# Kernel tuning notes

Hardware: AMD Instinct MI355X
Metric: run time of the kernel (lower is better)

The kernel has to match this reference:

```python
import jax, jax.numpy as jnp
import numpy as np

WEIGHT = 1e-7
SIGMA_RGB = 15.0
SIGMA_XY = 100.0
SCALE = 0.5


def _nearest_resize(x, Ho, Wo):
    # torch F.interpolate mode='nearest': src = floor(dst * in/out)
    H, W = x.shape[-2], x.shape[-1]
    iy = (jnp.arange(Ho) * (H / Ho)).astype(jnp.int32)
    ix = (jnp.arange(Wo) * (W / Wo)).astype(jnp.int32)
    return x[..., iy[:, None], ix[None, :]]


def _bilinear_resize(x, Ho, Wo):
    # torch bilinear, align_corners=False (half-pixel centers, no antialias)
    H, W = x.shape[-2], x.shape[-1]
    yc = jnp.clip((jnp.arange(Ho, dtype=jnp.float32) + 0.5) * (H / Ho) - 0.5, 0.0, H - 1.0)
    xc = jnp.clip((jnp.arange(Wo, dtype=jnp.float32) + 0.5) * (W / Wo) - 0.5, 0.0, W - 1.0)
    y0 = jnp.floor(yc).astype(jnp.int32); y1 = jnp.minimum(y0 + 1, H - 1); ty = yc - y0
    x0 = jnp.floor(xc).astype(jnp.int32); x1 = jnp.minimum(x0 + 1, W - 1); tx = xc - x0
    g = lambda yi, xi: x[..., yi[:, None], xi[None, :]]
    top = g(y0, x0) * (1.0 - tx) + g(y0, x1) * tx
    bot = g(y1, x0) * (1.0 - tx) + g(y1, x1) * tx
    return top * (1.0 - ty[:, None]) + bot * ty[:, None]


def _dense_energy(images, segmentations, ROIs, seg_label):
    N, K, H, W = segmentations.shape
    Ho, Wo = int(H * SCALE), int(W * SCALE)
    P = Ho * Wo
    img_s = _nearest_resize(images, Ho, Wo)            # [N,3,Ho,Wo]
    seg_s = _bilinear_resize(segmentations, Ho, Wo)    # [N,K,Ho,Wo]
    roi_s = _nearest_resize(ROIs, Ho, Wo)              # [N,Ho,Wo]
    lbl_s = _nearest_resize(seg_label, Ho, Wo)         # [N,1,Ho,Wo]
    unlabel = (lbl_s == 255)[:, 0]                     # [N,Ho,Wo]

    # Gate = clamp(ROI - max_k seg, min=0), with unlabeled region forced to 1
    gate = roi_s - jnp.max(seg_s, axis=1)
    gate = jnp.where(unlabel, 1.0, gate)
    gate = jnp.maximum(gate, 0.0)
    gate = jax.lax.stop_gradient(gate)                 # constant in the custom backward

    seg_roi = seg_s * roi_s[:, None]                   # [N,K,Ho,Wo]

    sxy = SIGMA_XY * SCALE
    yy, xx = jnp.meshgrid(jnp.arange(Ho, dtype=jnp.float32),
                          jnp.arange(Wo, dtype=jnp.float32), indexing='ij')
    pos = jnp.stack([xx.ravel() / sxy, yy.ravel() / sxy], axis=-1)  # [P,2]

    def per_image(img, seg):
        # img [3,Ho,Wo], seg [K,Ho,Wo] -> AS [K,P]: Gaussian bilateral filter
        col = img.reshape(img.shape[0], P).T / SIGMA_RGB            # [P,3]
        f = jnp.concatenate([pos, col], axis=-1)                    # [P,5]
        sq = jnp.sum(f * f, axis=-1)
        d2 = jnp.maximum(sq[:, None] + sq[None, :] - 2.0 * (f @ f.T), 0.0)
        Wm = jnp.exp(-0.5 * d2)                                     # [P,P] affinity
        return seg.reshape(seg.shape[0], P) @ Wm                    # symmetric Wm

    AS = jax.vmap(per_image)(img_s, seg_roi)                        # [N,K,P]
    AS = AS * gate.reshape(N, 1, P)
    loss = -jnp.sum(seg_roi.reshape(N, K, P) * AS) / N
    return (WEIGHT * loss).reshape(1)


def setup_inputs() -> dict:
    key = jax.random.key(0)
    k1, k2, k3, k4 = jax.random.split(key, 4)
    N, C, K, H, W = 4, 3, 21, 128, 128
    images = jax.random.uniform(k1, (N, C, H, W), dtype=jnp.float32) * 255.0
    segmentations = jax.nn.softmax(jax.random.normal(k2, (N, K, H, W), dtype=jnp.float32), axis=1)
    ROIs = jax.random.randint(k3, (N, H, W), 0, 2).astype(jnp.float32)
    seg_label = jax.random.randint(k4, (N, 1, H, W), 0, 256).astype(jnp.int32)
    return {"images": images, "segmentations": segmentations, "ROIs": ROIs, "seg_label": seg_label}


def reference(images, segmentations, ROIs, seg_label):
    return _dense_energy(images, segmentations, ROIs, seg_label)
```

## Files before the change

kernel.cpp:

```cpp
#include <hip/hip_runtime.h>
#include <hip/hip_bf16.h>


typedef _Float16 v8h __attribute__((ext_vector_type(8)));
typedef float v16f __attribute__((ext_vector_type(16)));

#define NIMG 4
#define KCH 21
#define HIN 128
#define WIN 128
#define PPX 4096

#define SG_OFF   0x000000
#define SR_OFF   0x0C0000
#define FT_OFF   0x180000
#define SQ_OFF   0x200000
#define PART_OFF 0x210000

#define CEXP -0.72134752044448170f
#define M2C   1.44269504088896341f

__device__ __forceinline__ float fexp2(float x) {
#if __has_builtin(__builtin_amdgcn_exp2f)
    return __builtin_amdgcn_exp2f(x);
#else
    return __expf(x * 0.69314718055994531f);
#endif
}

__global__ __launch_bounds__(256) void prep_kernel(
    const float* __restrict__ img, const float* __restrict__ seg,
    const float* __restrict__ roi, const int* __restrict__ lbl,
    char* __restrict__ ws)
{
    int gid = blockIdx.x * 256 + threadIdx.x;
    int n = gid >> 12, p = gid & (PPX - 1);
    int y = p >> 6, x = p & 63, iy = 2 * y, ix = 2 * x;
    const float inv_rgb = 1.0f / 15.0f, inv_sxy = 1.0f / 50.0f;

    float rv = roi[((size_t)n * HIN + iy) * WIN + ix];
    int   lb = lbl[((size_t)n * HIN + iy) * WIN + ix];

    float sv[KCH]; float maxs = 0.0f;
    #pragma unroll
    for (int k = 0; k < KCH; k++) {
        const float* sp = seg + ((((size_t)n * KCH + k) * HIN + iy) * WIN + ix);
        float2 a = *(const float2*)sp;
        float2 c = *(const float2*)(sp + WIN);
        float s = 0.25f * (a.x + a.y + c.x + c.y);
        maxs = fmaxf(maxs, s);
        sv[k] = s * rv;
    }
    float gate = (lb == 255) ? 1.0f : fmaxf(rv - maxs, 0.0f);

    union { v8h h[3]; _Float16 e[24]; } rr, gg;
    #pragma unroll
    for (int k = 0; k < KCH; k++) {
        rr.e[k] = (_Float16)sv[k];
        gg.e[k] = (_Float16)(sv[k] * gate);
    }
    #pragma unroll
    for (int k = KCH; k < 24; k++) { rr.e[k] = (_Float16)0.f; gg.e[k] = (_Float16)0.f; }

    v8h* sgp = (v8h*)(ws + SG_OFF + (size_t)gid * 48);
    v8h* srp = (v8h*)(ws + SR_OFF + (size_t)gid * 48);
    sgp[0] = gg.h[0]; sgp[1] = gg.h[1]; sgp[2] = gg.h[2];
    srp[0] = rr.h[0]; srp[1] = rr.h[1]; srp[2] = rr.h[2];

    float f[5];
    f[0] = (float)x * inv_sxy;
    f[1] = (float)y * inv_sxy;
    f[2] = img[(((size_t)n * 3 + 0) * HIN + iy) * WIN + ix] * inv_rgb;
    f[3] = img[(((size_t)n * 3 + 1) * HIN + iy) * WIN + ix] * inv_rgb;
    f[4] = img[(((size_t)n * 3 + 2) * HIN + iy) * WIN + ix] * inv_rgb;

    union { v8h h[2]; _Float16 e[16]; } ff;
    float sq = 0.f;
    #pragma unroll
    for (int i = 0; i < 5; i++) {
        _Float16 hi = (_Float16)f[i];
        _Float16 lo = (_Float16)(f[i] - (float)hi);
        ff.e[i] = hi; ff.e[8 + i] = lo;
        float fe = (float)hi + (float)lo;
        sq = fmaf(fe, fe, sq);
    }
    #pragma unroll
    for (int i = 5; i < 8; i++) { ff.e[i] = (_Float16)0.f; ff.e[8 + i] = (_Float16)0.f; }

    v8h* ftp = (v8h*)(ws + FT_OFF + (size_t)gid * 32);
    ftp[0] = ff.h[0]; ftp[1] = ff.h[1];
    *(float*)(ws + SQ_OFF + (size_t)gid * 4) = CEXP * sq;
}

#define QS_O 0
#define QF_O 9216
#define QQ_O 14336
#define PS_O 14848
#define PF_O 24064
#define PQ_O 29184
#define RED_O 29696
#define LDS_BYTES 29712

__global__ __launch_bounds__(256) void pairs_kernel(
    const char* __restrict__ ws, float* __restrict__ part)
{
    __shared__ __align__(16) char smem[LDS_BYTES];
    int b = blockIdx.x;
    int ps = b & 7, qt = (b >> 3) & 31, n = b >> 8;
    int t = threadIdx.x;
    int lane = t & 63, half = lane >> 5, lr = lane & 31, wv = t >> 6;
    int wq = wv & 1, wp = wv >> 1;

    const float* SGg = (const float*)(ws + SG_OFF);
    const float* SRg = (const float*)(ws + SR_OFF);
    const float* FTg = (const float*)(ws + FT_OFF);
    const float* SQg = (const float*)(ws + SQ_OFF);

    if (t < 128) {
        *(float2*)(smem + QS_O + t * 72 + 48) = make_float2(0.f, 0.f);
        *(float2*)(smem + QS_O + t * 72 + 56) = make_float2(0.f, 0.f);
        *(float2*)(smem + PS_O + t * 72 + 48) = make_float2(0.f, 0.f);
        *(float2*)(smem + PS_O + t * 72 + 56) = make_float2(0.f, 0.f);
    }

    {
        int qbase = n * PPX + qt * 128;
        const float* gS = SRg + (size_t)qbase * 12;
        #pragma unroll
        for (int i = 0; i < 6; i++) {
            int d = t + i * 256;
            int row = d / 12, off = d - row * 12;
            *(float*)(smem + QS_O + row * 72 + off * 4) = gS[d];
        }
        const float* gF = FTg + (size_t)qbase * 8;
        #pragma unroll
        for (int i = 0; i < 4; i++) {
            int d = t + i * 256;
            int row = d >> 3, off = d & 7;
            *(float*)(smem + QF_O + row * 40 + off * 4) = gF[d];
        }
        if (t < 128) *(float*)(smem + QQ_O + t * 4) = SQg[qbase + t];
    }
    __syncthreads();

    v8h BS[2][2], BFH[2], BFL[2]; float sqq[2];
    #pragma unroll
    for (int s = 0; s < 2; s++) {
        int cr = wq * 64 + s * 32 + lr;
        const char* rb = smem + QS_O + cr * 72 + half * 16;
        union { v8h h; float2 f[2]; } u0, u1, uh, ul;
        u0.f[0] = *(const float2*)(rb);        u0.f[1] = *(const float2*)(rb + 8);
        u1.f[0] = *(const float2*)(rb + 32);   u1.f[1] = *(const float2*)(rb + 40);
        const char* fb = smem + QF_O + cr * 40;
        uh.f[0] = *(const float2*)(fb);        uh.f[1] = *(const float2*)(fb + 8);
        ul.f[0] = *(const float2*)(fb + 16);   ul.f[1] = *(const float2*)(fb + 24);
        BS[s][0] = u0.h; BS[s][1] = u1.h; BFH[s] = uh.h; BFL[s] = ul.h;
        sqq[s] = *(const float*)(smem + QQ_O + cr * 4);
    }

    float a0c = 0.f, a1c = 0.f, a2c = 0.f, a3c = 0.f;
    int pbase0 = n * PPX + ps * 512;

    for (int ch = 0; ch < 4; ch++) {
        __syncthreads();
        int pbase = pbase0 + ch * 128;
        const float* gS = SGg + (size_t)pbase * 12;
        #pragma unroll
        for (int i = 0; i < 6; i++) {
            int d = t + i * 256;
            int row = d / 12, off = d - row * 12;
            *(float*)(smem + PS_O + row * 72 + off * 4) = gS[d];
        }
        const float* gF = FTg + (size_t)pbase * 8;
        #pragma unroll
        for (int i = 0; i < 4; i++) {
            int d = t + i * 256;
            int row = d >> 3, off = d & 7;
            *(float*)(smem + PF_O + row * 40 + off * 4) = gF[d];
        }
        if (t < 128) *(float*)(smem + PQ_O + t * 4) = SQg[pbase + t];
        __syncthreads();

        #pragma unroll
        for (int sp = 0; sp < 2; sp++) {
            int pr = wp * 64 + sp * 32 + lr;
            union { v8h h; float2 f[2]; } a0, a1, af;
            const char* rb = smem + PS_O + pr * 72 + half * 16;
            a0.f[0] = *(const float2*)(rb);        a0.f[1] = *(const float2*)(rb + 8);
            a1.f[0] = *(const float2*)(rb + 32);   a1.f[1] = *(const float2*)(rb + 40);
            const char* fb2 = smem + PF_O + pr * 40 + half * 16;
            af.f[0] = *(const float2*)(fb2);       af.f[1] = *(const float2*)(fb2 + 8);

            float sqp[16];
            int pr0 = wp * 64 + sp * 32 + half * 4;
            #pragma unroll
            for (int r = 0; r < 16; r++) {
                int row = pr0 + (r & 3) + 8 * (r >> 2);
                sqp[r] = *(const float*)(smem + PQ_O + row * 4);
            }

            #pragma unroll
            for (int s = 0; s < 2; s++) {
                v16f z = {0.f,0.f,0.f,0.f,0.f,0.f,0.f,0.f,0.f,0.f,0.f,0.f,0.f,0.f,0.f,0.f};
                v16f c2 = __builtin_amdgcn_mfma_f32_32x32x16_f16(af.h, BFH[s], z, 0, 0, 0);
                c2 = __builtin_amdgcn_mfma_f32_32x32x16_f16(af.h, BFL[s], c2, 0, 0, 0);
                v16f c1 = __builtin_amdgcn_mfma_f32_32x32x16_f16(a0.h, BS[s][0], z, 0, 0, 0);
                c1 = __builtin_amdgcn_mfma_f32_32x32x16_f16(a1.h, BS[s][1], c1, 0, 0, 0);
                float sqv = sqq[s];
                #pragma unroll
                for (int r = 0; r < 16; r++) {
                    float arg = fmaf(M2C, c2[r], sqp[r] + sqv);
                    arg = fminf(arg, 0.0f);
                    float w = fexp2(arg);
                    float v = w * c1[r];
                    if ((r & 3) == 0) a0c += v;
                    else if ((r & 3) == 1) a1c += v;
                    else if ((r & 3) == 2) a2c += v;
                    else a3c += v;
                }
            }
        }
    }

    float acc = (a0c + a1c) + (a2c + a3c);
    #pragma unroll
    for (int off = 32; off > 0; off >>= 1) acc += __shfl_down(acc, off, 64);
    float* wred = (float*)(smem + RED_O);
    if ((t & 63) == 0) wred[t >> 6] = acc;
    __syncthreads();
    if (t == 0)
        part[blockIdx.x] = (wred[0] + wred[1]) + (wred[2] + wred[3]);
}

__global__ __launch_bounds__(256) void finalize_kernel(
    const float* __restrict__ part, float* __restrict__ out)
{
    __shared__ float s[256];
    int t = threadIdx.x;
    float v = ((part[t] + part[t + 256]) + (part[t + 512] + part[t + 768]));
    s[t] = v;
    __syncthreads();
    #pragma unroll
    for (int off = 128; off > 0; off >>= 1) {
        if (t < off) s[t] += s[t + off];
        __syncthreads();
    }
    if (t == 0) out[0] = s[0] * (-1e-7f / (float)NIMG);
}

extern "C" void kernel_launch(void* const* d_in, const int* in_sizes, int n_in,
                              void* d_out, int out_size, void* d_ws, size_t ws_size,
                              hipStream_t stream) {
    const float* images = (const float*)d_in[0];
    const float* seg    = (const float*)d_in[1];
    const float* rois   = (const float*)d_in[2];
    const int*   lbl    = (const int*)d_in[3];
    float* out = (float*)d_out;
    char*  ws  = (char*)d_ws;
    float* part = (float*)(ws + PART_OFF);

    hipLaunchKernelGGL(prep_kernel, dim3((NIMG * PPX) / 256), dim3(256), 0, stream,
                       images, seg, rois, lbl, ws);
    hipLaunchKernelGGL(pairs_kernel, dim3(NIMG * 32 * 8), dim3(256), 0, stream,
                       (const char*)ws, part);
    hipLaunchKernelGGL(finalize_kernel, dim3(1), dim3(256), 0, stream,
                       (const float*)part, out);
}
```

Measured before the change: 90.74 us.

## Exploit affinity symmetry with upper-triangular tiles and fuse final reduction

The pairs kernel now walks only the upper-triangular 128x128 tile pairs of the symmetric affinity matrix. The gate factor is moved inside the sum as (g_p + g_q), and diagonal tiles are halved, which cuts exp and MFMA work roughly in half. Prep writes one packed 128-byte record per pixel instead of separate gated and ungated segmentation arrays. The separate finalize kernel is replaced by a last-block-done atomic counter reduction. The cost is more LDS per block, a triangular index loop per block, and reliance on counter-based cross-block synchronization.

```diff
diff --git a/kernel.cpp b/kernel.cpp
--- a/kernel.cpp
+++ b/kernel.cpp
@@ -10,12 +10,12 @@
 #define HIN 128
 #define WIN 128
 #define PPX 4096
-
-#define SG_OFF   0x000000
-#define SR_OFF   0x0C0000
-#define FT_OFF   0x180000
-#define SQ_OFF   0x200000
-#define PART_OFF 0x210000
+#define TPB 32
+#define TRI 528
+#define NBLK (NIMG * TRI)
+
+#define PART_OFF 0x200000
+#define CNT_OFF  0x202200
 
 #define CEXP -0.72134752044448170f
 #define M2C   1.44269504088896341f
@@ -34,6 +34,7 @@
     char* __restrict__ ws)
 {
     int gid = blockIdx.x * 256 + threadIdx.x;
+    if (gid == 0) *(unsigned*)(ws + CNT_OFF) = 0u;
     int n = gid >> 12, p = gid & (PPX - 1);
     int y = p >> 6, x = p & 63, iy = 2 * y, ix = 2 * x;
     const float inv_rgb = 1.0f / 15.0f, inv_sxy = 1.0f / 50.0f;
@@ -41,7 +42,9 @@
     float rv = roi[((size_t)n * HIN + iy) * WIN + ix];
     int   lb = lbl[((size_t)n * HIN + iy) * WIN + ix];
 
-    float sv[KCH]; float maxs = 0.0f;
+    union { float4 q[8]; float f[32]; _Float16 e[64]; } rec;
+
+    float maxs = 0.0f;
     #pragma unroll
     for (int k = 0; k < KCH; k++) {
         const float* sp = seg + ((((size_t)n * KCH + k) * HIN + iy) * WIN + ix);
@@ -49,23 +52,12 @@
         float2 c = *(const float2*)(sp + WIN);
         float s = 0.25f * (a.x + a.y + c.x + c.y);
         maxs = fmaxf(maxs, s);
-        sv[k] = s * rv;
-    }
+        rec.e[k] = (_Float16)(s * rv);
+    }
+    #pragma unroll
+    for (int k = KCH; k < 32; k++) rec.e[k] = (_Float16)0.f;
+
     float gate = (lb == 255) ? 1.0f : fmaxf(rv - maxs, 0.0f);
-
-    union { v8h h[3]; _Float16 e[24]; } rr, gg;
-    #pragma unroll
-    for (int k = 0; k < KCH; k++) {
-        rr.e[k] = (_Float16)sv[k];
-        gg.e[k] = (_Float16)(sv[k] * gate);
-    }
-    #pragma unroll
-    for (int k = KCH; k < 24; k++) { rr.e[k] = (_Float16)0.f; gg.e[k] = (_Float16)0.f; }
-
-    v8h* sgp = (v8h*)(ws + SG_OFF + (size_t)gid * 48);
-    v8h* srp = (v8h*)(ws + SR_OFF + (size_t)gid * 48);
-    sgp[0] = gg.h[0]; sgp[1] = gg.h[1]; sgp[2] = gg.h[2];
-    srp[0] = rr.h[0]; srp[1] = rr.h[1]; srp[2] = rr.h[2];
 
     float f[5];
     f[0] = (float)x * inv_sxy;
@@ -74,150 +66,137 @@
     f[3] = img[(((size_t)n * 3 + 1) * HIN + iy) * WIN + ix] * inv_rgb;
     f[4] = img[(((size_t)n * 3 + 2) * HIN + iy) * WIN + ix] * inv_rgb;
 
-    union { v8h h[2]; _Float16 e[16]; } ff;
     float sq = 0.f;
     #pragma unroll
     for (int i = 0; i < 5; i++) {
         _Float16 hi = (_Float16)f[i];
         _Float16 lo = (_Float16)(f[i] - (float)hi);
-        ff.e[i] = hi; ff.e[8 + i] = lo;
+        rec.e[32 + i] = hi; rec.e[40 + i] = lo;
         float fe = (float)hi + (float)lo;
         sq = fmaf(fe, fe, sq);
     }
     #pragma unroll
-    for (int i = 5; i < 8; i++) { ff.e[i] = (_Float16)0.f; ff.e[8 + i] = (_Float16)0.f; }
-
-    v8h* ftp = (v8h*)(ws + FT_OFF + (size_t)gid * 32);
-    ftp[0] = ff.h[0]; ftp[1] = ff.h[1];
-    *(float*)(ws + SQ_OFF + (size_t)gid * 4) = CEXP * sq;
-}
-
-#define QS_O 0
-#define QF_O 9216
-#define QQ_O 14336
-#define PS_O 14848
-#define PF_O 24064
-#define PQ_O 29184
-#define RED_O 29696
-#define LDS_BYTES 29712
-
-__global__ __launch_bounds__(256) void pairs_kernel(
-    const char* __restrict__ ws, float* __restrict__ part)
+    for (int i = 5; i < 8; i++) { rec.e[32 + i] = (_Float16)0.f; rec.e[40 + i] = (_Float16)0.f; }
+
+    rec.f[24] = CEXP * sq;
+    rec.f[25] = gate;
+    rec.f[26] = 0.f; rec.f[27] = 0.f;
+    rec.f[28] = 0.f; rec.f[29] = 0.f; rec.f[30] = 0.f; rec.f[31] = 0.f;
+
+    float4* dst = (float4*)(ws + (size_t)gid * 128);
+    #pragma unroll
+    for (int u = 0; u < 8; u++) dst[u] = rec.q[u];
+}
+
+#define LSTR 136
+#define RED_O  34816
+#define FLAG_O 34832
+#define LDS_BYTES 34848
+
+__global__ __launch_bounds__(256, 4) void pairs_kernel(
+    const char* __restrict__ ws, float* __restrict__ part,
+    unsigned* __restrict__ cnt, float* __restrict__ out)
 {
     __shared__ __align__(16) char smem[LDS_BYTES];
     int b = blockIdx.x;
-    int ps = b & 7, qt = (b >> 3) & 31, n = b >> 8;
+    int n = b / TRI, r = b - n * TRI;
+    int i = 0, rowlen = TPB;
+    while (r >= rowlen) { r -= rowlen; rowlen--; i++; }
+    int j = i + r;
+    bool diag = (i == j);
+
     int t = threadIdx.x;
     int lane = t & 63, half = lane >> 5, lr = lane & 31, wv = t >> 6;
     int wq = wv & 1, wp = wv >> 1;
 
-    const float* SGg = (const float*)(ws + SG_OFF);
-    const float* SRg = (const float*)(ws + SR_OFF);
-    const float* FTg = (const float*)(ws + FT_OFF);
-    const float* SQg = (const float*)(ws + SQ_OFF);
-
-    if (t < 128) {
-        *(float2*)(smem + QS_O + t * 72 + 48) = make_float2(0.f, 0.f);
-        *(float2*)(smem + QS_O + t * 72 + 56) = make_float2(0.f, 0.f);
-        *(float2*)(smem + PS_O + t * 72 + 48) = make_float2(0.f, 0.f);
-        *(float2*)(smem + PS_O + t * 72 + 56) = make_float2(0.f, 0.f);
-    }
-
+    const float4* recs = (const float4*)ws;
     {
-        int qbase = n * PPX + qt * 128;
-        const float* gS = SRg + (size_t)qbase * 12;
-        #pragma unroll
-        for (int i = 0; i < 6; i++) {
-            int d = t + i * 256;
-            int row = d / 12, off = d - row * 12;
-            *(float*)(smem + QS_O + row * 72 + off * 4) = gS[d];
-        }
-        const float* gF = FTg + (size_t)qbase * 8;
-        #pragma unroll
-        for (int i = 0; i < 4; i++) {
-            int d = t + i * 256;
-            int row = d >> 3, off = d & 7;
-            *(float*)(smem + QF_O + row * 40 + off * 4) = gF[d];
-        }
-        if (t < 128) *(float*)(smem + QQ_O + t * 4) = SQg[qbase + t];
+        int ibase = (n * PPX + i * 128) * 8;
+        #pragma unroll
+        for (int k = 0; k < 4; k++) {
+            int v = t + k * 256;
+            int row = v >> 3, off = v & 7;
+            float4 val = recs[ibase + v];
+            char* d = smem + row * LSTR + off * 16;
+            *(float2*)d = make_float2(val.x, val.y);
+            *(float2*)(d + 8) = make_float2(val.z, val.w);
+        }
+        if (!diag) {
+            int jbase = (n * PPX + j * 128) * 8;
+            #pragma unroll
+            for (int k = 0; k < 4; k++) {
+                int v = t + k * 256;
+                int row = v >> 3, off = v & 7;
+                float4 val = recs[jbase + v];
+                char* d = smem + (128 + row) * LSTR + off * 16;
+                *(float2*)d = make_float2(val.x, val.y);
+                *(float2*)(d + 8) = make_float2(val.z, val.w);
+            }
+        }
     }
     __syncthreads();
 
-    v8h BS[2][2], BFH[2], BFL[2]; float sqq[2];
+    int jrow0 = diag ? 0 : 128;
+
+    v8h BS[2][2], BFh[2], BFl[2]; float sqq[2], gq[2];
     #pragma unroll
     for (int s = 0; s < 2; s++) {
-        int cr = wq * 64 + s * 32 + lr;
-        const char* rb = smem + QS_O + cr * 72 + half * 16;
+        int cr = jrow0 + wq * 64 + s * 32 + lr;
+        const char* rb = smem + cr * LSTR;
         union { v8h h; float2 f[2]; } u0, u1, uh, ul;
-        u0.f[0] = *(const float2*)(rb);        u0.f[1] = *(const float2*)(rb + 8);
-        u1.f[0] = *(const float2*)(rb + 32);   u1.f[1] = *(const float2*)(rb + 40);
-        const char* fb = smem + QF_O + cr * 40;
-        uh.f[0] = *(const float2*)(fb);        uh.f[1] = *(const float2*)(fb + 8);
-        ul.f[0] = *(const float2*)(fb + 16);   ul.f[1] = *(const float2*)(fb + 24);
-        BS[s][0] = u0.h; BS[s][1] = u1.h; BFH[s] = uh.h; BFL[s] = ul.h;
-        sqq[s] = *(const float*)(smem + QQ_O + cr * 4);
+        u0.f[0] = *(const float2*)(rb + half * 16);
+        u0.f[1] = *(const float2*)(rb + half * 16 + 8);
+        u1.f[0] = *(const float2*)(rb + 32 + half * 16);
+        u1.f[1] = *(const float2*)(rb + 32 + half * 16 + 8);
+        uh.f[0] = *(const float2*)(rb + 64);  uh.f[1] = *(const float2*)(rb + 72);
+        ul.f[0] = *(const float2*)(rb + 80);  ul.f[1] = *(const float2*)(rb + 88);
+        BS[s][0] = u0.h; BS[s][1] = u1.h; BFh[s] = uh.h; BFl[s] = ul.h;
+        sqq[s] = *(const float*)(rb + 96);
+        gq[s]  = *(const float*)(rb + 100);
     }
 
     float a0c = 0.f, a1c = 0.f, a2c = 0.f, a3c = 0.f;
-    int pbase0 = n * PPX + ps * 512;
-
-    for (int ch = 0; ch < 4; ch++) {
-        __syncthreads();
-        int pbase = pbase0 + ch * 128;
-        const float* gS = SGg + (size_t)pbase * 12;
-        #pragma unroll
-        for (int i = 0; i < 6; i++) {
-            int d = t + i * 256;
-            int row = d / 12, off = d - row * 12;
-            *(float*)(smem + PS_O + row * 72 + off * 4) = gS[d];
-        }
-        const float* gF = FTg + (size_t)pbase * 8;
-        #pragma unroll
-        for (int i = 0; i < 4; i++) {
-            int d = t + i * 256;
-            int row = d >> 3, off = d & 7;
-            *(float*)(smem + PF_O + row * 40 + off * 4) = gF[d];
-        }
-        if (t < 128) *(float*)(smem + PQ_O + t * 4) = SQg[pbase + t];
-        __syncthreads();
-
-        #pragma unroll
-        for (int sp = 0; sp < 2; sp++) {
-            int pr = wp * 64 + sp * 32 + lr;
-            union { v8h h; float2 f[2]; } a0, a1, af;
-            const char* rb = smem + PS_O + pr * 72 + half * 16;
-            a0.f[0] = *(const float2*)(rb);        a0.f[1] = *(const float2*)(rb + 8);
-            a1.f[0] = *(const float2*)(rb + 32);   a1.f[1] = *(const float2*)(rb + 40);
-            const char* fb2 = smem + PF_O + pr * 40 + half * 16;
-            af.f[0] = *(const float2*)(fb2);       af.f[1] = *(const float2*)(fb2 + 8);
-
-            float sqp[16];
-            int pr0 = wp * 64 + sp * 32 + half * 4;
+
+    #pragma unroll
+    for (int sp = 0; sp < 2; sp++) {
+        int pr = wp * 64 + sp * 32 + lr;
+        const char* rb = smem + pr * LSTR;
+        union { v8h h; float2 f[2]; } a0, a1, af;
+        a0.f[0] = *(const float2*)(rb + half * 16);
+        a0.f[1] = *(const float2*)(rb + half * 16 + 8);
+        a1.f[0] = *(const float2*)(rb + 32 + half * 16);
+        a1.f[1] = *(const float2*)(rb + 32 + half * 16 + 8);
+        af.f[0] = *(const float2*)(rb + 64 + half * 16);
+        af.f[1] = *(const float2*)(rb + 64 + half * 16 + 8);
+
+        float sqp[16], gp[16];
+        int pr0 = wp * 64 + sp * 32 + half * 4;
+        #pragma unroll
+        for (int rr = 0; rr < 16; rr++) {
+            int row = pr0 + (rr & 3) + 8 * (rr >> 2);
+            sqp[rr] = *(const float*)(smem + row * LSTR + 96);
+            gp[rr]  = *(const float*)(smem + row * LSTR + 100);
+        }
+
+        #pragma unroll
+        for (int s = 0; s < 2; s++) {
+            v16f z = {0.f,0.f,0.f,0.f,0.f,0.f,0.f,0.f,0.f,0.f,0.f,0.f,0.f,0.f,0.f,0.f};
+            v16f c2 = __builtin_amdgcn_mfma_f32_32x32x16_f16(af.h, BFh[s], z, 0, 0, 0);
+            c2 = __builtin_amdgcn_mfma_f32_32x32x16_f16(af.h, BFl[s], c2, 0, 0, 0);
+            v16f c1 = __builtin_amdgcn_mfma_f32_32x32x16_f16(a0.h, BS[s][0], z, 0, 0, 0);
+            c1 = __builtin_amdgcn_mfma_f32_32x32x16_f16(a1.h, BS[s][1], c1, 0, 0, 0);
+            float sqv = sqq[s], gv = gq[s];
             #pragma unroll
-            for (int r = 0; r < 16; r++) {
-                int row = pr0 + (r & 3) + 8 * (r >> 2);
-                sqp[r] = *(const float*)(smem + PQ_O + row * 4);
-            }
-
-            #pragma unroll
-            for (int s = 0; s < 2; s++) {
-                v16f z = {0.f,0.f,0.f,0.f,0.f,0.f,0.f,0.f,0.f,0.f,0.f,0.f,0.f,0.f,0.f,0.f};
-                v16f c2 = __builtin_amdgcn_mfma_f32_32x32x16_f16(af.h, BFH[s], z, 0, 0, 0);
-                c2 = __builtin_amdgcn_mfma_f32_32x32x16_f16(af.h, BFL[s], c2, 0, 0, 0);
-                v16f c1 = __builtin_amdgcn_mfma_f32_32x32x16_f16(a0.h, BS[s][0], z, 0, 0, 0);
-                c1 = __builtin_amdgcn_mfma_f32_32x32x16_f16(a1.h, BS[s][1], c1, 0, 0, 0);
-                float sqv = sqq[s];
-                #pragma unroll
-                for (int r = 0; r < 16; r++) {
-                    float arg = fmaf(M2C, c2[r], sqp[r] + sqv);
-                    arg = fminf(arg, 0.0f);
-                    float w = fexp2(arg);
-                    float v = w * c1[r];
-                    if ((r & 3) == 0) a0c += v;
-                    else if ((r & 3) == 1) a1c += v;
-                    else if ((r & 3) == 2) a2c += v;
-                    else a3c += v;
-                }
+            for (int rr = 0; rr < 16; rr++) {
+                float arg = fmaf(M2C, c2[rr], sqp[rr] + sqv);
+                arg = fminf(arg, 0.0f);
+                float w = fexp2(arg);
+                float v = w * c1[rr];
+                float gg = gp[rr] + gv;
+                if ((rr & 3) == 0)      a0c = fmaf(gg, v, a0c);
+                else if ((rr & 3) == 1) a1c = fmaf(gg, v, a1c);
+                else if ((rr & 3) == 2) a2c = fmaf(gg, v, a2c);
+                else                    a3c = fmaf(gg, v, a3c);
             }
         }
     }
@@ -226,26 +205,39 @@
     #pragma unroll
     for (int off = 32; off > 0; off >>= 1) acc += __shfl_down(acc, off, 64);
     float* wred = (float*)(smem + RED_O);
+    int* flag = (int*)(smem + FLAG_O);
     if ((t & 63) == 0) wred[t >> 6] = acc;
     __syncthreads();
-    if (t == 0)
-        part[blockIdx.x] = (wred[0] + wred[1]) + (wred[2] + wred[3]);
-}
-
-__global__ __launch_bounds__(256) void finalize_kernel(
-    const float* __restrict__ part, float* __restrict__ out)
-{
-    __shared__ float s[256];
-    int t = threadIdx.x;
-    float v = ((part[t] + part[t + 256]) + (part[t + 512] + part[t + 768]));
-    s[t] = v;
+    if (t == 0) {
+        float partial = (wred[0] + wred[1]) + (wred[2] + wred[3]);
+        if (diag) partial *= 0.5f;
+        part[b] = partial;
+        __threadfence();
+        unsigned old = atomicAdd(cnt, 1u);
+        *flag = (old == NBLK - 1) ? 1 : 0;
+    }
     __syncthreads();
-    #pragma unroll
-    for (int off = 128; off > 0; off >>= 1) {
-        if (t < off) s[t] += s[t + off];
+
+    if (*flag) {
+        __threadfence();
+        float v = 0.f;
+        #pragma unroll
+        for (int k = 0; k < 9; k++) {
+            int idx = t + k * 256;
+            if (idx < NBLK)
+                v += __hip_atomic_load(&part[idx], __ATOMIC_RELAXED,
+                                       __HIP_MEMORY_SCOPE_AGENT);
+        }
+        float* red = (float*)smem;
+        red[t] = v;
         __syncthreads();
-    }
-    if (t == 0) out[0] = s[0] * (-1e-7f / (float)NIMG);
+        #pragma unroll
+        for (int off = 128; off > 0; off >>= 1) {
+            if (t < off) red[t] += red[t + off];
+            __syncthreads();
+        }
+        if (t == 0) out[0] = red[0] * (-1e-7f / (float)NIMG);
+    }
 }
 
 extern "C" void kernel_launch(void* const* d_in, const int* in_sizes, int n_in,
@@ -258,11 +250,10 @@
     float* out = (float*)d_out;
     char*  ws  = (char*)d_ws;
     float* part = (float*)(ws + PART_OFF);
+    unsigned* cnt = (unsigned*)(ws + CNT_OFF);
 
     hipLaunchKernelGGL(prep_kernel, dim3((NIMG * PPX) / 256), dim3(256), 0, stream,
                        images, seg, rois, lbl, ws);
-    hipLaunchKernelGGL(pairs_kernel, dim3(NIMG * 32 * 8), dim3(256), 0, stream,
-                       (const char*)ws, part);
-    hipLaunchKernelGGL(finalize_kernel, dim3(1), dim3(256), 0, stream,
-                       (const float*)part, out);
-}
+    hipLaunchKernelGGL(pairs_kernel, dim3(NBLK), dim3(256), 0, stream,
+                       (const char*)ws, part, cnt, out);
+}
```

New measurement: 141.6 us. 56.0% more time.
